# Kernel optimization log

Measured on AMD Instinct MI355X. Metric: run time of the kernel, lower is better.

The kernel has to match this reference:

```python
import jax, jax.numpy as jnp
import numpy as np

N_NODES = 30000
N_EDGES = 480000
N_GRAPHS = 512
NUM_NEIGHBORS = 3.8
DIM_SH = 16       # l=0..3 spherical harmonics
DIM_GATE_IN = 160 # 16x0e+16x0o + 8x0e+8x0o+8x0e+8x0o + 16x1o+16x1e
DIM_GATE_OUT = 128
DIM_OUT = 7       # 0o + 6x0e


def spherical_harmonics_l3(u):
    # real spherical harmonics l=0..3, 'component' normalization (|Y_l|^2 ~ 2l+1)
    x, y, z = u[:, 0], u[:, 1], u[:, 2]
    x2, y2, z2 = x * x, y * y, z * z
    sh = [
        jnp.ones_like(x),
        3 ** 0.5 * x, 3 ** 0.5 * y, 3 ** 0.5 * z,
        15 ** 0.5 * x * y, 15 ** 0.5 * y * z,
        (5 ** 0.5 / 2) * (3 * z2 - 1),
        15 ** 0.5 * x * z,
        (15 ** 0.5 / 2) * (x2 - y2),
        (35 / 8) ** 0.5 * y * (3 * x2 - y2),
        105 ** 0.5 * x * y * z,
        (21 / 8) ** 0.5 * y * (5 * z2 - 1),
        (7 ** 0.5 / 2) * z * (5 * z2 - 3),
        (21 / 8) ** 0.5 * x * (5 * z2 - 1),
        (105 ** 0.5 / 2) * z * (x2 - y2),
        (35 / 8) ** 0.5 * x * (x2 - y2),
    ]
    return jnp.stack(sh, axis=-1)  # [E, 16]


def radial_embed(r):
    # soft_one_hot_linspace(start=0.5, end=2.5, number=3, basis='smooth_finite', cutoff=True) * sqrt(3)
    values = jnp.array([0.5, 1.5, 2.5], dtype=r.dtype)
    u = r[:, None] - values          # step = 1.0
    d = u * u - 1.0
    c = 1.14136 * np.exp(2.0)
    emb = jnp.where(d < 0, c * jnp.exp(1.0 / jnp.where(d < 0, d, -1.0)), 0.0)
    return emb * 3 ** 0.5            # [E, 3]


def mlp(s, W1, W2):
    # FullyConnectedNet([3, 256, K], relu): no bias, fan-in normalized
    h = jax.nn.relu(s @ (W1 / 3 ** 0.5))
    return h @ (W2 / 256 ** 0.5)


def conv(nf, edge_src, edge_dst, sh, w, cg, n_nodes):
    # gather -> per-edge weighted CG bilinear product -> scatter-add
    xs = nf[edge_src]                      # [E, Din]
    K, Din, Dsh = cg.shape
    E = xs.shape[0]
    if Din * Dsh <= 512:
        outer = (xs[:, :, None] * sh[:, None, :]).reshape(E, Din * Dsh)
        ef = outer @ cg.reshape(K, Din * Dsh).T           # [E, K]
    else:
        t = jnp.einsum('ei,kij->ekj', xs, cg)             # [E, K, Dsh] (K small)
        ef = jnp.einsum('ekj,ej->ek', t, sh)
    ef = ef * w                                           # per-edge learned weights
    out = jax.ops.segment_sum(ef, edge_dst, num_segments=n_nodes)
    return out / NUM_NEIGHBORS ** 0.5


def gate(x):
    # Gate('16x0e+16x0o', [relu, abs], '8x0e+8x0o+8x0e+8x0o', [relu,tanh,relu,tanh], '16x1o+16x1e')
    n = x.shape[0]
    s = jnp.concatenate([jax.nn.relu(x[:, :16]), jnp.abs(x[:, 16:32])], axis=1)
    g = jnp.concatenate([
        jax.nn.relu(x[:, 32:40]), jnp.tanh(x[:, 40:48]),
        jax.nn.relu(x[:, 48:56]), jnp.tanh(x[:, 56:64]),
    ], axis=1)                                            # [n, 32]
    vec = x[:, 64:160].reshape(n, 32, 3)                  # 16x1o + 16x1e
    gated = (vec * g[:, :, None]).reshape(n, 96)
    return jnp.concatenate([s, gated], axis=1)            # [n, 128]


def setup_inputs() -> dict:
    key = jax.random.key(0)
    ks = jax.random.split(key, 10)
    pos = jax.random.normal(ks[0], (N_NODES, 3), dtype=jnp.float32)
    edge_src = jax.random.randint(ks[1], (N_EDGES,), 0, N_NODES)
    edge_dst = jax.random.randint(ks[2], (N_EDGES,), 0, N_NODES)
    batch = jnp.sort(jax.random.randint(ks[3], (N_NODES,), 0, N_GRAPHS))
    W1a = jax.random.normal(ks[4], (3, 256), dtype=jnp.float32)
    W2a = jax.random.normal(ks[5], (256, DIM_GATE_IN), dtype=jnp.float32)
    cg1 = jax.random.normal(ks[6], (DIM_GATE_IN, DIM_SH, DIM_SH), dtype=jnp.float32) / DIM_SH
    W1b = jax.random.normal(ks[7], (3, 256), dtype=jnp.float32)
    W2b = jax.random.normal(ks[8], (256, DIM_OUT), dtype=jnp.float32)
    cg2 = jax.random.normal(ks[9], (DIM_OUT, DIM_GATE_OUT, DIM_SH), dtype=jnp.float32) / DIM_SH
    return {"pos": pos, "W1a": W1a, "W2a": W2a, "cg1": cg1, "W1b": W1b,
            "W2b": W2b, "cg2": cg2, "edge_src": edge_src, "edge_dst": edge_dst,
            "batch": batch}


def reference(pos, W1a, W2a, cg1, W1b, W2b, cg2, edge_src, edge_dst, batch):
    ev = pos[edge_src] - pos[edge_dst]                    # [E, 3]
    r = jnp.linalg.norm(ev, axis=1)
    u = ev / jnp.maximum(r, 1e-9)[:, None]
    sh = spherical_harmonics_l3(u)                        # [E, 16]
    scal = radial_embed(r)                                # [E, 3]

    # initial node features: scatter of edge attributes
    x = jax.ops.segment_sum(sh, edge_dst, num_segments=N_NODES) / NUM_NEIGHBORS ** 0.5

    w1 = mlp(scal, W1a, W2a)                              # [E, 160]
    x = conv(x, edge_src, edge_dst, sh, w1, cg1, N_NODES) # [N, 160]
    x = gate(x)                                           # [N, 128]
    w2 = mlp(scal, W1b, W2b)                              # [E, 7]
    x = conv(x, edge_src, edge_dst, sh, w2, cg2, N_NODES) # [N, 7]

    out = jax.ops.segment_sum(x, batch, num_segments=N_GRAPHS) / 4 ** 0.5
    return out                                            # [512, 7]
```

## Files before the change

### kernel.cpp

```cpp
#include <hip/hip_runtime.h>
#include <math.h>

#define NN 30000
#define NE 480000
#define NG 512

#define INV_SQRT_NN 0.5129891760425771f
#define INV_SQRT3   0.5773502691896258f
#define SCALE_W2    0.0625f
#define RAD_C       14.607377f

typedef __bf16 bf16x8 __attribute__((ext_vector_type(8)));
typedef float f32x4 __attribute__((ext_vector_type(4)));
typedef unsigned short ushort8 __attribute__((ext_vector_type(8)));

__device__ __forceinline__ unsigned short f2bf(float f) {
  unsigned int u = __float_as_uint(f);
  return (unsigned short)((u + 0x7FFFu + ((u >> 16) & 1u)) >> 16);
}

__global__ __launch_bounds__(256) void k_edge(
    const float* __restrict__ pos,
    const int* __restrict__ esrc,
    const int* __restrict__ edst,
    float* __restrict__ shg,
    float* __restrict__ scalg,
    float* __restrict__ x0) {
  __shared__ float S_lds[256*17];
  __shared__ int   d_lds[256];
  const int t = threadIdx.x;
  const int e = blockIdx.x * 256 + t;
  int s = esrc[e], d = edst[e];
  float ex = pos[3*s]   - pos[3*d];
  float ey = pos[3*s+1] - pos[3*d+1];
  float ez = pos[3*s+2] - pos[3*d+2];
  float r = sqrtf(ex*ex + ey*ey + ez*ez);
  float inv = 1.0f / fmaxf(r, 1e-9f);
  float x = ex*inv, y = ey*inv, z = ez*inv;
  float x2 = x*x, y2 = y*y, z2 = z*z;
  float S[16];
  S[0]  = 1.0f;
  S[1]  = 1.7320508075688772f * x;
  S[2]  = 1.7320508075688772f * y;
  S[3]  = 1.7320508075688772f * z;
  S[4]  = 3.872983346207417f * x * y;
  S[5]  = 3.872983346207417f * y * z;
  S[6]  = 1.118033988749895f * (3.0f*z2 - 1.0f);
  S[7]  = 3.872983346207417f * x * z;
  S[8]  = 1.9364916731037085f * (x2 - y2);
  S[9]  = 2.091650066335189f  * y * (3.0f*x2 - y2);
  S[10] = 10.246950765959598f * x * y * z;
  S[11] = 1.6201851746019651f * y * (5.0f*z2 - 1.0f);
  S[12] = 1.3228756555322954f * z * (5.0f*z2 - 3.0f);
  S[13] = 1.6201851746019651f * x * (5.0f*z2 - 1.0f);
  S[14] = 5.123475382979799f  * z * (x2 - y2);
  S[15] = 2.091650066335189f  * x * (x2 - y2);
  float4* shv = (float4*)(shg + (size_t)e * 16);
  shv[0] = make_float4(S[0],  S[1],  S[2],  S[3]);
  shv[1] = make_float4(S[4],  S[5],  S[6],  S[7]);
  shv[2] = make_float4(S[8],  S[9],  S[10], S[11]);
  shv[3] = make_float4(S[12], S[13], S[14], S[15]);
  float sc[3];
  #pragma unroll
  for (int c = 0; c < 3; ++c) {
    float v = 0.5f + (float)c;
    float uu = r - v;
    float dd = uu*uu - 1.0f;
    sc[c] = (dd < 0.0f) ? RAD_C * expf(1.0f/dd) : 0.0f;
  }
  ((float4*)scalg)[e] = make_float4(sc[0], sc[1], sc[2], 0.0f);

  d_lds[t] = d;
  #pragma unroll
  for (int j = 0; j < 16; ++j) S_lds[t*17 + j] = S[j];
  __syncthreads();
  #pragma unroll
  for (int it = 0; it < 16; ++it) {
    int idx = it*256 + t;
    int el = idx >> 4, j = idx & 15;
    atomicAdd(&x0[(size_t)d_lds[el]*16 + j], S_lds[el*17 + j]);
  }
}

__global__ void k_prep(const float* __restrict__ W2a, const float* __restrict__ cg1,
                       const float* __restrict__ cg2, const float* __restrict__ W2b,
                       unsigned short* __restrict__ Bcg, unsigned short* __restrict__ Bw2,
                       unsigned short* __restrict__ Bc2, unsigned short* __restrict__ Bw2b) {
  int tid = blockIdx.x * 256 + threadIdx.x;
  if (tid >= 12544) return;
  if (tid < 10240) {
    int sel = tid >= 5120;
    int t = sel ? tid - 5120 : tid;
    int lane = t & 63;
    int kc = (t >> 6) & 7;
    int nt = t >> 9;
    int n  = nt*16 + (lane & 15);
    int kb = kc*32 + (lane >> 4)*8;
    ushort8 v;
    if (!sel) {
      #pragma unroll
      for (int j = 0; j < 8; ++j) v[j] = f2bf(cg1[n*256 + kb + j]);
      *(ushort8*)&Bcg[(size_t)t*8] = v;
    } else {
      #pragma unroll
      for (int j = 0; j < 8; ++j) v[j] = f2bf(W2a[(kb + j)*160 + n] * SCALE_W2);
      *(ushort8*)&Bw2[(size_t)t*8] = v;
    }
  } else if (tid < 12032) {
    int et = tid - 10240;
    int L = et & 63;
    int kc = (et >> 6) & 3;
    int nt = et >> 8;
    int mcol = L & 15;
    int ib = kc*32 + (L >> 4)*8;
    ushort8 v;
    #pragma unroll
    for (int jj = 0; jj < 8; ++jj) v[jj] = f2bf(cg2[nt*2048 + (ib + jj)*16 + mcol]);
    *(ushort8*)&Bc2[(size_t)et*8] = v;
  } else {
    int et = tid - 12032;
    int L = et & 63;
    int kc = et >> 6;
    int mcol = L & 15;
    int ib = kc*32 + (L >> 4)*8;
    ushort8 v;
    #pragma unroll
    for (int jj = 0; jj < 8; ++jj)
      v[jj] = (mcol < 7) ? f2bf(W2b[(ib + jj)*7 + mcol] * SCALE_W2) : (unsigned short)0;
    *(ushort8*)&Bw2b[(size_t)et*8] = v;
  }
}

__global__ __launch_bounds__(256, 2) void k_conv1(
    const float* __restrict__ x0, const float* __restrict__ shg,
    const float* __restrict__ scalg,
    const int* __restrict__ esrc, const int* __restrict__ edst,
    const float* __restrict__ W1a,
    const unsigned short* __restrict__ Bcg, const unsigned short* __restrict__ Bw2,
    float* __restrict__ x1) {
  __shared__ float sh_lds[64*20];
  __shared__ float xs_lds[64*20];
  __shared__ unsigned short Bpan[2][20*512];
  const int t = threadIdx.x;
  const int e0 = blockIdx.x * 64;

  {
    int e = t >> 2, q = t & 3;
    int ge = e0 + e;
    *(float4*)&sh_lds[e*20 + q*4] = ((const float4*)shg)[(size_t)ge*4 + q];
    float4 xv = ((const float4*)x0)[(size_t)esrc[ge]*4 + q];
    xv.x *= INV_SQRT_NN; xv.y *= INV_SQRT_NN; xv.z *= INV_SQRT_NN; xv.w *= INV_SQRT_NN;
    *(float4*)&xs_lds[e*20 + q*4] = xv;
  }
  const int L  = t & 63;
  const int wv = t >> 6;
  const int m  = L & 15;
  const int q4 = L >> 4;
  const int j0 = (q4 & 1) * 8;
  const int p  = q4 >> 1;
  const int el = wv*16 + m;

  const unsigned short* psrc[5];
  unsigned short* pdst0[5];
  #pragma unroll
  for (int i = 0; i < 5; ++i) {
    int pnl = wv*5 + i;
    int g = pnl >= 10;
    int nt = g ? pnl - 10 : pnl;
    psrc[i] = (g ? Bw2 : Bcg) + (((size_t)nt*8)*64 + L)*8;
    pdst0[i] = &Bpan[0][pnl*512 + L*8];
  }

  float4 sc = ((const float4*)scalg)[e0 + el];
  const float hs0 = sc.x*INV_SQRT3, hs1 = sc.y*INV_SQRT3, hs2 = sc.z*INV_SQRT3;

  ushort8 pf[5];
  #pragma unroll
  for (int i = 0; i < 5; ++i) pf[i] = *(const ushort8*)psrc[i];
  #pragma unroll
  for (int i = 0; i < 5; ++i) *(ushort8*)pdst0[i] = pf[i];
  __syncthreads();

  float sh8[8];
  *(float4*)&sh8[0] = *(float4*)&sh_lds[el*20 + j0];
  *(float4*)&sh8[4] = *(float4*)&sh_lds[el*20 + j0 + 4];
  float xsc[8];
  #pragma unroll
  for (int kc = 0; kc < 8; ++kc) xsc[kc] = xs_lds[el*20 + kc*2 + p];

  f32x4 ac[10], aw[10];
  #pragma unroll
  for (int i = 0; i < 10; ++i) {
    ac[i] = (f32x4)(0.0f);
    aw[i] = (f32x4)(0.0f);
  }

  #pragma unroll
  for (int kc = 0; kc < 8; ++kc) {
    if (kc < 7) {
      #pragma unroll
      for (int i = 0; i < 5; ++i) pf[i] = *(const ushort8*)(psrc[i] + (size_t)(kc+1)*512);
    }
    float xc = xsc[kc];
    ushort8 ao;
    #pragma unroll
    for (int j = 0; j < 8; ++j) ao[j] = f2bf(xc * sh8[j]);
    int mh = kc*32 + q4*8;
    float4 w0a = *(const float4*)&W1a[mh];
    float4 w0b = *(const float4*)&W1a[mh + 4];
    float4 w1a = *(const float4*)&W1a[256 + mh];
    float4 w1b = *(const float4*)&W1a[256 + mh + 4];
    float4 w2a = *(const float4*)&W1a[512 + mh];
    float4 w2b = *(const float4*)&W1a[512 + mh + 4];
    ushort8 ah;
    ah[0] = f2bf(fmaxf(hs0*w0a.x + hs1*w1a.x + hs2*w2a.x, 0.0f));
    ah[1] = f2bf(fmaxf(hs0*w0a.y + hs1*w1a.y + hs2*w2a.y, 0.0f));
    ah[2] = f2bf(fmaxf(hs0*w0a.z + hs1*w1a.z + hs2*w2a.z, 0.0f));
    ah[3] = f2bf(fmaxf(hs0*w0a.w + hs1*w1a.w + hs2*w2a.w, 0.0f));
    ah[4] = f2bf(fmaxf(hs0*w0b.x + hs1*w1b.x + hs2*w2b.x, 0.0f));
    ah[5] = f2bf(fmaxf(hs0*w0b.y + hs1*w1b.y + hs2*w2b.y, 0.0f));
    ah[6] = f2bf(fmaxf(hs0*w0b.z + hs1*w1b.z + hs2*w2b.z, 0.0f));
    ah[7] = f2bf(fmaxf(hs0*w0b.w + hs1*w1b.w + hs2*w2b.w, 0.0f));
    bf16x8 aoB = __builtin_bit_cast(bf16x8, ao);
    bf16x8 ahB = __builtin_bit_cast(bf16x8, ah);
    const unsigned short* buf = &Bpan[kc & 1][0];
    #pragma unroll
    for (int nt = 0; nt < 10; ++nt) {
      ushort8 b1 = *(const ushort8*)&buf[nt*512 + L*8];
      ushort8 b2 = *(const ushort8*)&buf[(10 + nt)*512 + L*8];
      ac[nt] = __builtin_amdgcn_mfma_f32_16x16x32_bf16(aoB, __builtin_bit_cast(bf16x8, b1), ac[nt], 0, 0, 0);
      aw[nt] = __builtin_amdgcn_mfma_f32_16x16x32_bf16(ahB, __builtin_bit_cast(bf16x8, b2), aw[nt], 0, 0, 0);
    }
    if (kc < 7) {
      unsigned short* dst = &Bpan[(kc + 1) & 1][0];
      #pragma unroll
      for (int i = 0; i < 5; ++i) *(ushort8*)(dst + (wv*5 + i)*512 + L*8) = pf[i];
      __syncthreads();
    }
  }

  int ebase = e0 + wv*16 + q4*4;
  int d0 = edst[ebase], d1 = edst[ebase+1], d2 = edst[ebase+2], d3 = edst[ebase+3];
  #pragma unroll
  for (int nt = 0; nt < 10; ++nt) {
    int col = nt*16 + m;
    atomicAdd(&x1[(size_t)d0*160 + col], ac[nt][0]*aw[nt][0]*INV_SQRT_NN);
    atomicAdd(&x1[(size_t)d1*160 + col], ac[nt][1]*aw[nt][1]*INV_SQRT_NN);
    atomicAdd(&x1[(size_t)d2*160 + col], ac[nt][2]*aw[nt][2]*INV_SQRT_NN);
    atomicAdd(&x1[(size_t)d3*160 + col], ac[nt][3]*aw[nt][3]*INV_SQRT_NN);
  }
}

__device__ __forceinline__ float gate_val(const float* xr, int o) {
  if (o < 16) return fmaxf(xr[o], 0.0f);
  if (o < 32) return fabsf(xr[o]);
  int oo = o - 32;
  int vi = oo / 3;
  float g = xr[32 + vi];
  g = (vi & 8) ? tanhf(g) : fmaxf(g, 0.0f);
  return xr[64 + oo] * g;
}

__global__ void k_gate(const float* __restrict__ x1, unsigned short* __restrict__ x2b) {
  int tid = blockIdx.x * 256 + threadIdx.x;
  if (tid >= NN*64) return;
  int n = tid >> 6, o2 = (tid & 63) * 2;
  const float* xr = x1 + (size_t)n * 160;
  ushort2 st;
  st.x = f2bf(gate_val(xr, o2));
  st.y = f2bf(gate_val(xr, o2 + 1));
  *(ushort2*)&x2b[(size_t)n*128 + o2] = st;
}

__global__ __launch_bounds__(256, 2) void k_conv2(
    const unsigned short* __restrict__ x2b, const float* __restrict__ shg,
    const float* __restrict__ scalg,
    const int* __restrict__ esrc, const int* __restrict__ edst,
    const float* __restrict__ W1b,
    const unsigned short* __restrict__ Bc2, const unsigned short* __restrict__ Bw2b,
    float* __restrict__ x3) {
  __shared__ float sh_lds[128*20];
  const int t = threadIdx.x;
  const int e0 = blockIdx.x * 128;
  #pragma unroll
  for (int i = 0; i < 2; ++i) {
    int idx = t + 256*i;
    int e = idx >> 2, q = idx & 3;
    *(float4*)&sh_lds[e*20 + q*4] = ((const float4*)shg)[(size_t)(e0 + e)*4 + q];
  }
  __syncthreads();

  const int L = t & 63, wv = t >> 6;
  const int m = L & 15, q4 = L >> 4;
  const int el0 = wv*32 + m;
  const int el1 = el0 + 16;
  const int s0 = esrc[e0 + el0];
  const int s1 = esrc[e0 + el1];
  float4 scA = ((const float4*)scalg)[e0 + el0];
  float4 scB = ((const float4*)scalg)[e0 + el1];
  const float hsA0 = scA.x*INV_SQRT3, hsA1 = scA.y*INV_SQRT3, hsA2 = scA.z*INV_SQRT3;
  const float hsB0 = scB.x*INV_SQRT3, hsB1 = scB.y*INV_SQRT3, hsB2 = scB.z*INV_SQRT3;

  f32x4 tAcc[2][7];
  #pragma unroll
  for (int tt = 0; tt < 2; ++tt)
    #pragma unroll
    for (int nt = 0; nt < 7; ++nt) tAcc[tt][nt] = (f32x4)(0.0f);
  f32x4 wAcc[2];
  wAcc[0] = (f32x4)(0.0f); wAcc[1] = (f32x4)(0.0f);

  const unsigned short* arow0 = x2b + (size_t)s0*128 + q4*8;
  const unsigned short* arow1 = x2b + (size_t)s1*128 + q4*8;
  #pragma unroll
  for (int kc = 0; kc < 4; ++kc) {
    ushort8 a0 = *(const ushort8*)&arow0[kc*32];
    ushort8 a1 = *(const ushort8*)&arow1[kc*32];
    bf16x8 a0B = __builtin_bit_cast(bf16x8, a0);
    bf16x8 a1B = __builtin_bit_cast(bf16x8, a1);
    #pragma unroll
    for (int nt = 0; nt < 7; ++nt) {
      ushort8 b = *(const ushort8*)&Bc2[(((size_t)nt*4 + kc)*64 + L)*8];
      bf16x8 bB = __builtin_bit_cast(bf16x8, b);
      tAcc[0][nt] = __builtin_amdgcn_mfma_f32_16x16x32_bf16(a0B, bB, tAcc[0][nt], 0, 0, 0);
      tAcc[1][nt] = __builtin_amdgcn_mfma_f32_16x16x32_bf16(a1B, bB, tAcc[1][nt], 0, 0, 0);
    }
  }
  #pragma unroll
  for (int kc = 0; kc < 8; ++kc) {
    int mh = kc*32 + q4*8;
    float4 w0a = *(const float4*)&W1b[mh];
    float4 w0b = *(const float4*)&W1b[mh + 4];
    float4 w1a = *(const float4*)&W1b[256 + mh];
    float4 w1b = *(const float4*)&W1b[256 + mh + 4];
    float4 w2a = *(const float4*)&W1b[512 + mh];
    float4 w2b = *(const float4*)&W1b[512 + mh + 4];
    ushort8 ahA, ahB;
    ahA[0] = f2bf(fmaxf(hsA0*w0a.x + hsA1*w1a.x + hsA2*w2a.x, 0.0f));
    ahA[1] = f2bf(fmaxf(hsA0*w0a.y + hsA1*w1a.y + hsA2*w2a.y, 0.0f));
    ahA[2] = f2bf(fmaxf(hsA0*w0a.z + hsA1*w1a.z + hsA2*w2a.z, 0.0f));
    ahA[3] = f2bf(fmaxf(hsA0*w0a.w + hsA1*w1a.w + hsA2*w2a.w, 0.0f));
    ahA[4] = f2bf(fmaxf(hsA0*w0b.x + hsA1*w1b.x + hsA2*w2b.x, 0.0f));
    ahA[5] = f2bf(fmaxf(hsA0*w0b.y + hsA1*w1b.y + hsA2*w2b.y, 0.0f));
    ahA[6] = f2bf(fmaxf(hsA0*w0b.z + hsA1*w1b.z + hsA2*w2b.z, 0.0f));
    ahA[7] = f2bf(fmaxf(hsA0*w0b.w + hsA1*w1b.w + hsA2*w2b.w, 0.0f));
    ahB[0] = f2bf(fmaxf(hsB0*w0a.x + hsB1*w1a.x + hsB2*w2a.x, 0.0f));
    ahB[1] = f2bf(fmaxf(hsB0*w0a.y + hsB1*w1a.y + hsB2*w2a.y, 0.0f));
    ahB[2] = f2bf(fmaxf(hsB0*w0a.z + hsB1*w1a.z + hsB2*w2a.z, 0.0f));
    ahB[3] = f2bf(fmaxf(hsB0*w0a.w + hsB1*w1a.w + hsB2*w2a.w, 0.0f));
    ahB[4] = f2bf(fmaxf(hsB0*w0b.x + hsB1*w1b.x + hsB2*w2b.x, 0.0f));
    ahB[5] = f2bf(fmaxf(hsB0*w0b.y + hsB1*w1b.y + hsB2*w2b.y, 0.0f));
    ahB[6] = f2bf(fmaxf(hsB0*w0b.z + hsB1*w1b.z + hsB2*w2b.z, 0.0f));
    ahB[7] = f2bf(fmaxf(hsB0*w0b.w + hsB1*w1b.w + hsB2*w2b.w, 0.0f));
    ushort8 b = *(const ushort8*)&Bw2b[((size_t)kc*64 + L)*8];
    bf16x8 bB = __builtin_bit_cast(bf16x8, b);
    wAcc[0] = __builtin_amdgcn_mfma_f32_16x16x32_bf16(__builtin_bit_cast(bf16x8, ahA), bB, wAcc[0], 0, 0, 0);
    wAcc[1] = __builtin_amdgcn_mfma_f32_16x16x32_bf16(__builtin_bit_cast(bf16x8, ahB), bB, wAcc[1], 0, 0, 0);
  }

  #pragma unroll
  for (int tt = 0; tt < 2; ++tt) {
    int base = wv*32 + tt*16 + q4*4;
    int dsts[4];
    #pragma unroll
    for (int r = 0; r < 4; ++r) dsts[r] = edst[e0 + base + r];
    float ef[4] = {0.f, 0.f, 0.f, 0.f};
    #pragma unroll
    for (int nt = 0; nt < 7; ++nt) {
      #pragma unroll
      for (int r = 0; r < 4; ++r) {
        float v = tAcc[tt][nt][r] * sh_lds[(base + r)*20 + m];
        v += __shfl_xor(v, 1);
        v += __shfl_xor(v, 2);
        v += __shfl_xor(v, 4);
        v += __shfl_xor(v, 8);
        if (m == nt) ef[r] = v;
      }
    }
    if (m < 7) {
      #pragma unroll
      for (int r = 0; r < 4; ++r)
        atomicAdd(&x3[(size_t)dsts[r]*7 + m], ef[r] * wAcc[tt][r] * INV_SQRT_NN);
    }
  }
}

__global__ void k_out(const float* __restrict__ x3, const int* __restrict__ batch,
                      float* __restrict__ out) {
  int tid = blockIdx.x * 256 + threadIdx.x;
  if (tid >= NN*7) return;
  int n = tid / 7;
  int k = tid - n*7;
  atomicAdd(&out[batch[n]*7 + k], x3[tid] * 0.5f);
}

extern "C" void kernel_launch(void* const* d_in, const int* in_sizes, int n_in,
                              void* d_out, int out_size, void* d_ws, size_t ws_size,
                              hipStream_t stream) {
  const float* pos  = (const float*)d_in[0];
  const float* W1a  = (const float*)d_in[1];
  const float* W2a  = (const float*)d_in[2];
  const float* cg1  = (const float*)d_in[3];
  const float* W1b  = (const float*)d_in[4];
  const float* W2b  = (const float*)d_in[5];
  const float* cg2  = (const float*)d_in[6];
  const int* esrc   = (const int*)d_in[7];
  const int* edst   = (const int*)d_in[8];
  const int* batch  = (const int*)d_in[9];
  float* out = (float*)d_out;

  float* ws    = (float*)d_ws;
  float* shg   = ws;
  float* scalg = shg   + (size_t)NE*16;
  float* x0    = scalg + (size_t)NE*4;
  float* x1    = x0    + (size_t)NN*16;
  float* x2g   = x1    + (size_t)NN*160;
  float* x3    = x2g   + (size_t)NN*128;
  unsigned short* x2b  = (unsigned short*)x2g;
  unsigned short* Bcg  = (unsigned short*)(x3 + (size_t)NN*7);
  unsigned short* Bw2  = Bcg + 40960;
  unsigned short* Bc2  = Bw2 + 40960;
  unsigned short* Bw2b = Bc2 + 14336;

  hipMemsetAsync(x0, 0, sizeof(float)*(size_t)NN*16, stream);
  hipMemsetAsync(x1, 0, sizeof(float)*(size_t)NN*160, stream);
  hipMemsetAsync(x3, 0, sizeof(float)*(size_t)NN*7, stream);
  hipMemsetAsync(d_out, 0, sizeof(float)*NG*7, stream);

  k_prep <<<49, 256, 0, stream>>>(W2a, cg1, cg2, W2b, Bcg, Bw2, Bc2, Bw2b);
  k_edge <<<NE/256, 256, 0, stream>>>(pos, esrc, edst, shg, scalg, x0);
  k_conv1<<<NE/64, 256, 0, stream>>>(x0, shg, scalg, esrc, edst, W1a, Bcg, Bw2, x1);
  k_gate <<<(NN*64)/256, 256, 0, stream>>>(x1, x2b);
  k_conv2<<<NE/128, 256, 0, stream>>>(x2b, shg, scalg, esrc, edst, W1b, Bc2, Bw2b, x3);
  k_out  <<<(NN*7 + 255)/256, 256, 0, stream>>>(x3, batch, out);
}
```

Before: 495.5 us.

## Sort edges by destination for conv1 and merge duplicate atomics

Adds a histogram and single-block scan, then a counting-sort permutation of edges by destination built inside k_edge. conv1 processes edges in destination-sorted order and combines the contributions of consecutive edges that share a destination before issuing the atomicAdd. The goal is to cut the number of scattered float atomics into the 160-wide x1 rows. In exchange it adds two kernels (one of which is a slow serial one-block scan), extra atomics in k_edge, and indirect gathers through perm in conv1.

```diff
diff --git a/kernel.cpp b/kernel.cpp
--- a/kernel.cpp
+++ b/kernel.cpp
@@ -17,6 +17,36 @@
 __device__ __forceinline__ unsigned short f2bf(float f) {
   unsigned int u = __float_as_uint(f);
   return (unsigned short)((u + 0x7FFFu + ((u >> 16) & 1u)) >> 16);
+}
+
+__global__ void k_hist(const int* __restrict__ edst, int* __restrict__ hist) {
+  int e = blockIdx.x * 256 + threadIdx.x;
+  if (e < NE) atomicAdd(&hist[edst[e]], 1);
+}
+
+__global__ __launch_bounds__(256) void k_scan(const int* __restrict__ hist,
+                                              int* __restrict__ cursor) {
+  __shared__ int partial[256];
+  const int CH = 118;
+  int t = threadIdx.x;
+  int base = t * CH;
+  int s = 0;
+  for (int i = 0; i < CH; ++i) {
+    int idx = base + i;
+    if (idx < NN) s += hist[idx];
+  }
+  partial[t] = s;
+  __syncthreads();
+  int pre = 0;
+  for (int i = 0; i < t; ++i) pre += partial[i];
+  int run = pre;
+  for (int i = 0; i < CH; ++i) {
+    int idx = base + i;
+    if (idx < NN) {
+      cursor[idx] = run;
+      run += hist[idx];
+    }
+  }
 }
 
 __global__ __launch_bounds__(256) void k_edge(
@@ -25,12 +55,18 @@
     const int* __restrict__ edst,
     float* __restrict__ shg,
     float* __restrict__ scalg,
-    float* __restrict__ x0) {
+    float* __restrict__ x0,
+    int* __restrict__ cursor,
+    int* __restrict__ perm,
+    int* __restrict__ dstS) {
   __shared__ float S_lds[256*17];
   __shared__ int   d_lds[256];
   const int t = threadIdx.x;
   const int e = blockIdx.x * 256 + t;
   int s = esrc[e], d = edst[e];
+  int ppos = atomicAdd(&cursor[d], 1);
+  perm[ppos] = e;
+  dstS[ppos] = d;
   float ex = pos[3*s]   - pos[3*d];
   float ey = pos[3*s+1] - pos[3*d+1];
   float ez = pos[3*s+2] - pos[3*d+2];
@@ -134,7 +170,8 @@
 __global__ __launch_bounds__(256, 2) void k_conv1(
     const float* __restrict__ x0, const float* __restrict__ shg,
     const float* __restrict__ scalg,
-    const int* __restrict__ esrc, const int* __restrict__ edst,
+    const int* __restrict__ esrc, const int* __restrict__ perm,
+    const int* __restrict__ dstS,
     const float* __restrict__ W1a,
     const unsigned short* __restrict__ Bcg, const unsigned short* __restrict__ Bw2,
     float* __restrict__ x1) {
@@ -146,7 +183,7 @@
 
   {
     int e = t >> 2, q = t & 3;
-    int ge = e0 + e;
+    int ge = perm[e0 + e];
     *(float4*)&sh_lds[e*20 + q*4] = ((const float4*)shg)[(size_t)ge*4 + q];
     float4 xv = ((const float4*)x0)[(size_t)esrc[ge]*4 + q];
     xv.x *= INV_SQRT_NN; xv.y *= INV_SQRT_NN; xv.z *= INV_SQRT_NN; xv.w *= INV_SQRT_NN;
@@ -171,7 +208,7 @@
     pdst0[i] = &Bpan[0][pnl*512 + L*8];
   }
 
-  float4 sc = ((const float4*)scalg)[e0 + el];
+  float4 sc = ((const float4*)scalg)[perm[e0 + el]];
   const float hs0 = sc.x*INV_SQRT3, hs1 = sc.y*INV_SQRT3, hs2 = sc.z*INV_SQRT3;
 
   ushort8 pf[5];
@@ -240,14 +277,22 @@
   }
 
   int ebase = e0 + wv*16 + q4*4;
-  int d0 = edst[ebase], d1 = edst[ebase+1], d2 = edst[ebase+2], d3 = edst[ebase+3];
+  int dd[4];
+  #pragma unroll
+  for (int r = 0; r < 4; ++r) dd[r] = dstS[ebase + r];
   #pragma unroll
   for (int nt = 0; nt < 10; ++nt) {
     int col = nt*16 + m;
-    atomicAdd(&x1[(size_t)d0*160 + col], ac[nt][0]*aw[nt][0]*INV_SQRT_NN);
-    atomicAdd(&x1[(size_t)d1*160 + col], ac[nt][1]*aw[nt][1]*INV_SQRT_NN);
-    atomicAdd(&x1[(size_t)d2*160 + col], ac[nt][2]*aw[nt][2]*INV_SQRT_NN);
-    atomicAdd(&x1[(size_t)d3*160 + col], ac[nt][3]*aw[nt][3]*INV_SQRT_NN);
+    float v0 = ac[nt][0]*aw[nt][0]*INV_SQRT_NN;
+    float v1 = ac[nt][1]*aw[nt][1]*INV_SQRT_NN;
+    float v2 = ac[nt][2]*aw[nt][2]*INV_SQRT_NN;
+    float v3 = ac[nt][3]*aw[nt][3]*INV_SQRT_NN;
+    float acc = v0;
+    int dp = dd[0];
+    if (dd[1] == dp) acc += v1; else { atomicAdd(&x1[(size_t)dp*160 + col], acc); acc = v1; dp = dd[1]; }
+    if (dd[2] == dp) acc += v2; else { atomicAdd(&x1[(size_t)dp*160 + col], acc); acc = v2; dp = dd[2]; }
+    if (dd[3] == dp) acc += v3; else { atomicAdd(&x1[(size_t)dp*160 + col], acc); acc = v3; dp = dd[3]; }
+    atomicAdd(&x1[(size_t)dp*160 + col], acc);
   }
 }
 
@@ -420,15 +465,22 @@
   unsigned short* Bw2  = Bcg + 40960;
   unsigned short* Bc2  = Bw2 + 40960;
   unsigned short* Bw2b = Bc2 + 14336;
+  int* hist   = (int*)(Bw2b + 4096);
+  int* cursor = hist + NN;
+  int* perm   = cursor + NN;
+  int* dstS   = perm + NE;
 
   hipMemsetAsync(x0, 0, sizeof(float)*(size_t)NN*16, stream);
   hipMemsetAsync(x1, 0, sizeof(float)*(size_t)NN*160, stream);
   hipMemsetAsync(x3, 0, sizeof(float)*(size_t)NN*7, stream);
   hipMemsetAsync(d_out, 0, sizeof(float)*NG*7, stream);
-
+  hipMemsetAsync(hist, 0, sizeof(int)*NN, stream);
+
+  k_hist <<<(NE + 255)/256, 256, 0, stream>>>(edst, hist);
+  k_scan <<<1, 256, 0, stream>>>(hist, cursor);
   k_prep <<<49, 256, 0, stream>>>(W2a, cg1, cg2, W2b, Bcg, Bw2, Bc2, Bw2b);
-  k_edge <<<NE/256, 256, 0, stream>>>(pos, esrc, edst, shg, scalg, x0);
-  k_conv1<<<NE/64, 256, 0, stream>>>(x0, shg, scalg, esrc, edst, W1a, Bcg, Bw2, x1);
+  k_edge <<<NE/256, 256, 0, stream>>>(pos, esrc, edst, shg, scalg, x0, cursor, perm, dstS);
+  k_conv1<<<NE/64, 256, 0, stream>>>(x0, shg, scalg, esrc, perm, dstS, W1a, Bcg, Bw2, x1);
   k_gate <<<(NN*64)/256, 256, 0, stream>>>(x1, x2b);
   k_conv2<<<NE/128, 256, 0, stream>>>(x2b, shg, scalg, esrc, edst, W1b, Bc2, Bw2b, x3);
   k_out  <<<(NN*7 + 255)/256, 256, 0, stream>>>(x3, batch, out);
```

After: 603.8 us. +21.9%, slower.
